# Performance work log

Hardware: AMD Instinct MI355X
Metric: run time of the kernel (lower is better)

Reference implementation:

```python
import jax, jax.numpy as jnp
import numpy as np

N, E, F_IN, HEADS, C_HEAD, HID, B, NCLS = 20000, 320000, 128, 2, 256, 512, 64, 38
EL = E + N  # edges with self-loops appended


def _bn(x, g, b, eps=1e-5):
    mu = jnp.mean(x, 0)
    var = jnp.mean((x - mu) ** 2, 0)
    return g * (x - mu) * jax.lax.rsqrt(var + eps) + b


def _gcn(x, W, b, src, dst):
    # src/dst already include self-loops; symmetric deg^-1/2 normalization (PyG GCNConv)
    h = x @ W                                             # [N, HID]
    deg = jax.ops.segment_sum(jnp.ones(EL, x.dtype), dst, N)
    norm = jax.lax.rsqrt(jnp.maximum(deg, 1.0))
    coef = norm[src] * norm[dst]                          # [EL]
    agg = jax.ops.segment_sum(h[src] * coef[:, None], dst, N)
    return agg + b


def _gat(x, W, a_src, a_dst, b, src, dst):
    # PyG GATConv, heads=2, concat: alpha = softmax_dst(leaky_relu(a_s.h_src + a_d.h_dst))
    h = (x @ W).reshape(N, HEADS, C_HEAD)
    as_n = jnp.sum(h * a_src, -1)                         # [N, HEADS]
    ad_n = jnp.sum(h * a_dst, -1)
    e = jax.nn.leaky_relu(as_n[src] + ad_n[dst], 0.2)     # [EL, HEADS]
    m = jax.ops.segment_max(e, dst, N)
    ex = jnp.exp(e - m[dst])
    s = jax.ops.segment_sum(ex, dst, N)
    alpha = ex / s[dst]                                   # [EL, HEADS]
    out = jax.ops.segment_sum(h[src] * alpha[:, :, None], dst, N)
    return out.reshape(N, HEADS * C_HEAD) + b


def setup_inputs() -> dict:
    key = jax.random.key(0)
    ks = jax.random.split(key, 40)
    x = jax.random.normal(ks[0], (N, F_IN), jnp.float32)
    edge_index = jax.random.randint(ks[1], (2, E), 0, N, jnp.int32)
    batch = jnp.sort(jax.random.randint(ks[2], (N,), 0, B, jnp.int32))

    def lin(k, fi, fo):
        bound = np.sqrt(6.0 / fi)
        return jax.random.uniform(k, (fi, fo), jnp.float32, -bound, bound)

    d = dict(x=x, edge_index=edge_index, batch=batch)
    # feature transform
    d['ft_W'] = lin(ks[3], F_IN, HID); d['ft_b'] = jnp.zeros(HID)
    d['ft_g'] = jnp.ones(HID); d['ft_be'] = jnp.zeros(HID)
    # GCN block
    d['gcn1_W'] = lin(ks[4], HID, HID); d['gcn1_b'] = jnp.zeros(HID)
    d['gbn1_g'] = jnp.ones(HID); d['gbn1_b'] = jnp.zeros(HID)
    d['gcn2_W'] = lin(ks[5], HID, HID); d['gcn2_b'] = jnp.zeros(HID)
    d['gbn2_g'] = jnp.ones(HID); d['gbn2_b'] = jnp.zeros(HID)
    # GAT block
    abound = np.sqrt(6.0 / HEADS)
    d['gat1_W'] = lin(ks[6], HID, HID)
    d['gat1_as'] = jax.random.uniform(ks[7], (HEADS, C_HEAD), jnp.float32, -abound, abound)
    d['gat1_ad'] = jax.random.uniform(ks[8], (HEADS, C_HEAD), jnp.float32, -abound, abound)
    d['gat1_b'] = jnp.zeros(HID)
    d['abn1_g'] = jnp.ones(HID); d['abn1_b'] = jnp.zeros(HID)
    d['gat2_W'] = lin(ks[9], HID, HID)
    d['gat2_as'] = jax.random.uniform(ks[10], (HEADS, C_HEAD), jnp.float32, -abound, abound)
    d['gat2_ad'] = jax.random.uniform(ks[11], (HEADS, C_HEAD), jnp.float32, -abound, abound)
    d['gat2_b'] = jnp.zeros(HID)
    d['abn2_g'] = jnp.ones(HID); d['abn2_b'] = jnp.zeros(HID)
    # classifier
    d['fc1_W'] = lin(ks[12], 2 * HID, HID); d['fc1_b'] = jnp.zeros(HID)
    d['cbn1_g'] = jnp.ones(HID); d['cbn1_b'] = jnp.zeros(HID)
    d['fc2_W'] = lin(ks[13], HID, HID // 2); d['fc2_b'] = jnp.zeros(HID // 2)
    d['cbn2_g'] = jnp.ones(HID // 2); d['cbn2_b'] = jnp.zeros(HID // 2)
    d['out_W'] = lin(ks[14], HID // 2, NCLS); d['out_b'] = jnp.zeros(NCLS)
    return d


def reference(x, edge_index, batch,
              ft_W, ft_b, ft_g, ft_be,
              gcn1_W, gcn1_b, gbn1_g, gbn1_b, gcn2_W, gcn2_b, gbn2_g, gbn2_b,
              gat1_W, gat1_as, gat1_ad, gat1_b, abn1_g, abn1_b,
              gat2_W, gat2_as, gat2_ad, gat2_b, abn2_g, abn2_b,
              fc1_W, fc1_b, cbn1_g, cbn1_b, fc2_W, fc2_b, cbn2_g, cbn2_b,
              out_W, out_b):
    loop = jnp.arange(N, dtype=edge_index.dtype)
    src = jnp.concatenate([edge_index[0], loop])
    dst = jnp.concatenate([edge_index[1], loop])

    # feature transform: Linear -> BN -> LeakyReLU(0.2)
    h = jax.nn.leaky_relu(_bn(x @ ft_W + ft_b, ft_g, ft_be), 0.2)
    # GCN block
    h = jax.nn.elu(_bn(_gcn(h, gcn1_W, gcn1_b, src, dst), gbn1_g, gbn1_b))
    h = jax.nn.elu(_bn(_gcn(h, gcn2_W, gcn2_b, src, dst), gbn2_g, gbn2_b))
    # GAT block
    h = jax.nn.elu(_bn(_gat(h, gat1_W, gat1_as, gat1_ad, gat1_b, src, dst), abn1_g, abn1_b))
    h = jax.nn.elu(_bn(_gat(h, gat2_W, gat2_as, gat2_ad, gat2_b, src, dst), abn2_g, abn2_b))
    # global mean+max pool over graphs
    cnt = jax.ops.segment_sum(jnp.ones(N, h.dtype), batch, B)
    mean_p = jax.ops.segment_sum(h, batch, B) / jnp.maximum(cnt, 1.0)[:, None]
    max_p = jax.ops.segment_max(h, batch, B)
    p = jnp.concatenate([mean_p, max_p], axis=1)           # [B, 1024]
    # classifier: fc1 -> bn -> fc2 -> bn -> leaky_relu -> out
    z = _bn(p @ fc1_W + fc1_b, cbn1_g, cbn1_b)
    z = _bn(z @ fc2_W + fc2_b, cbn2_g, cbn2_b)
    z = jax.nn.leaky_relu(z, 0.2)
    return z @ out_W + out_b                                # [B, NCLS]
```

## Files before the change

kernel.cpp:

```cpp
#include <hip/hip_runtime.h>

#define N_NODES 20000
#define N_EDGES 320000
#define EDG_ALL (N_EDGES + N_NODES)
#define F_IN 128
#define HID 512
#define NB 64
#define NCLS 38
#define M_PAD 20096
#define NBLK_SCAN ((N_NODES + 255) / 256)
#define BN_ROWS 16
#define BN_GRID ((N_NODES + BN_ROWS - 1) / BN_ROWS)
#define POOL_SPLIT 4

typedef short bf16x8 __attribute__((ext_vector_type(8)));
typedef float f32x4 __attribute__((ext_vector_type(4)));
typedef _Float16 f16;
typedef _Float16 f16x2 __attribute__((ext_vector_type(2)));

__device__ inline unsigned short f2bf(float f) {
  union { float f; unsigned u; } v; v.f = f;
  unsigned r = v.u + 0x7FFF + ((v.u >> 16) & 1);
  return (unsigned short)(r >> 16);
}

__device__ inline void split2(float f, unsigned short& h, unsigned short& l) {
  unsigned short hh = f2bf(f);
  union { unsigned u; float f; } vh; vh.u = ((unsigned)hh) << 16;
  h = hh;
  l = f2bf(f - vh.f);
}

__device__ inline void gload16(const void* g, void* l) {
  __builtin_amdgcn_global_load_lds(
      (const __attribute__((address_space(1))) unsigned int*)g,
      (__attribute__((address_space(3))) unsigned int*)l, 16, 0, 0);
}


__global__ void deg_count(const int* __restrict__ ei, int* __restrict__ deg) {
  int e = blockIdx.x * blockDim.x + threadIdx.x;
  if (e >= EDG_ALL) return;
  int d = (e < N_EDGES) ? ei[N_EDGES + e] : (e - N_EDGES);
  atomicAdd(&deg[d], 1);
}

__global__ void scan_p1(const int* __restrict__ deg, int* __restrict__ bsum) {
  __shared__ int sh[256];
  int b = blockIdx.x, t = threadIdx.x, i = b * 256 + t;
  sh[t] = (i < N_NODES) ? deg[i] : 0;
  __syncthreads();
  for (int o = 128; o > 0; o >>= 1) {
    if (t < o) sh[t] += sh[t + o];
    __syncthreads();
  }
  if (t == 0) bsum[b] = sh[0];
}

__global__ void scan_p2(const int* __restrict__ bsum, int* __restrict__ boff) {
  __shared__ int sh[128];
  int t = threadIdx.x;
  sh[t] = (t < NBLK_SCAN) ? bsum[t] : 0;
  __syncthreads();
  for (int o = 1; o < 128; o <<= 1) {
    int v = (t >= o) ? sh[t - o] : 0;
    __syncthreads();
    sh[t] += v;
    __syncthreads();
  }
  boff[t] = (t == 0) ? 0 : sh[t - 1];
}

__global__ void scan_p3(const int* __restrict__ deg, const int* __restrict__ boff,
                        int* __restrict__ row_ptr) {
  __shared__ int sh[256];
  int b = blockIdx.x, t = threadIdx.x, i = b * 256 + t;
  sh[t] = (i < N_NODES) ? deg[i] : 0;
  __syncthreads();
  for (int o = 1; o < 256; o <<= 1) {
    int v = (t >= o) ? sh[t - o] : 0;
    __syncthreads();
    sh[t] += v;
    __syncthreads();
  }
  if (i < N_NODES) row_ptr[i + 1] = boff[b] + sh[t];
  if (i == 0) row_ptr[0] = 0;
}

__global__ void compute_norm(const int* __restrict__ deg, float* __restrict__ norm) {
  int i = blockIdx.x * blockDim.x + threadIdx.x;
  if (i >= N_NODES) return;
  norm[i] = rsqrtf(fmaxf((float)deg[i], 1.f));
}

__global__ void fill_csr(const int* __restrict__ ei, int* __restrict__ cursor,
                         int* __restrict__ csr_src) {
  int e = blockIdx.x * blockDim.x + threadIdx.x;
  if (e >= EDG_ALL) return;
  int s, d;
  if (e < N_EDGES) { s = ei[e]; d = ei[N_EDGES + e]; }
  else { s = d = e - N_EDGES; }
  int pos = atomicAdd(&cursor[d], 1);
  csr_src[pos] = s;
}


__global__ void conv_split4(const float* __restrict__ in, unsigned short* __restrict__ hi,
                            unsigned short* __restrict__ lo, int n4) {
  int i = blockIdx.x * blockDim.x + threadIdx.x;
  if (i >= n4) return;
  float4 v = ((const float4*)in)[i];
  ushort4 h, l;
  split2(v.x, h.x, l.x); split2(v.y, h.y, l.y);
  split2(v.z, h.z, l.z); split2(v.w, h.w, l.w);
  ((ushort4*)hi)[i] = h;
  ((ushort4*)lo)[i] = l;
}

__global__ __launch_bounds__(256) void wtrans_split(const float* __restrict__ W,
                                                    unsigned short* __restrict__ WTh,
                                                    unsigned short* __restrict__ WTl,
                                                    int K, int N) {
  __shared__ float sh[32][33];
  int k0 = blockIdx.y * 32, n0 = blockIdx.x * 32;
  int r = threadIdx.x >> 5, c = threadIdx.x & 31;
#pragma unroll
  for (int i = 0; i < 4; ++i)
    sh[r + 8 * i][c] = W[(size_t)(k0 + r + 8 * i) * N + n0 + c];
  __syncthreads();
#pragma unroll
  for (int i = 0; i < 4; ++i) {
    unsigned short h, l;
    split2(sh[c][r + 8 * i], h, l);
    WTh[(size_t)(n0 + r + 8 * i) * K + k0 + c] = h;
    WTl[(size_t)(n0 + r + 8 * i) * K + k0 + c] = l;
  }
}

__global__ __launch_bounds__(256) void ftrans(const float* __restrict__ W,
                                              float* __restrict__ WT, int K, int N) {
  __shared__ float sh[32][33];
  int k0 = blockIdx.y * 32, n0 = blockIdx.x * 32;
  int r = threadIdx.x >> 5, c = threadIdx.x & 31;
#pragma unroll
  for (int i = 0; i < 4; ++i) {
    int k = k0 + r + 8 * i, n = n0 + c;
    sh[r + 8 * i][c] = (k < K && n < N) ? W[(size_t)k * N + n] : 0.f;
  }
  __syncthreads();
#pragma unroll
  for (int i = 0; i < 4; ++i) {
    int n = n0 + r + 8 * i, k = k0 + c;
    if (n < N && k < K) WT[(size_t)n * K + k] = sh[c][r + 8 * i];
  }
}


template <int K, typename OT>
__global__ __launch_bounds__(256) void mm_split(const unsigned short* __restrict__ Ah,
                                                const unsigned short* __restrict__ Al,
                                                const unsigned short* __restrict__ Bh,
                                                const unsigned short* __restrict__ Bl,
                                                const float* __restrict__ bias,
                                                OT* __restrict__ C) {
  __shared__ unsigned short AsH[4096], AsL[4096], BsH[4096], BsL[4096];
  const int t = threadIdx.x;
  const int wid = t >> 6, l = t & 63;
  const int row0 = blockIdx.y * 128;
  const int col0 = blockIdx.x * 128;
  const int wm = wid >> 1, wn = wid & 1;

  f32x4 acc[4][4];
#pragma unroll
  for (int m = 0; m < 4; ++m)
#pragma unroll
    for (int n = 0; n < 4; ++n)
#pragma unroll
      for (int q = 0; q < 4; ++q) acc[m][n][q] = 0.f;

  const size_t aoff = (size_t)(row0 + wid * 32 + (l >> 2)) * K + (l & 3) * 8;
  const size_t boff = (size_t)(col0 + wid * 32 + (l >> 2)) * K + (l & 3) * 8;
  const unsigned short* gAh0 = Ah + aoff; const unsigned short* gAh1 = gAh0 + (size_t)16 * K;
  const unsigned short* gAl0 = Al + aoff; const unsigned short* gAl1 = gAl0 + (size_t)16 * K;
  const unsigned short* gBh0 = Bh + boff; const unsigned short* gBh1 = gBh0 + (size_t)16 * K;
  const unsigned short* gBl0 = Bl + boff; const unsigned short* gBl1 = gBl0 + (size_t)16 * K;
  unsigned short* lAh0 = &AsH[(wid * 2 + 0) * 512];
  unsigned short* lAh1 = &AsH[(wid * 2 + 1) * 512];
  unsigned short* lAl0 = &AsL[(wid * 2 + 0) * 512];
  unsigned short* lAl1 = &AsL[(wid * 2 + 1) * 512];
  unsigned short* lBh0 = &BsH[(wid * 2 + 0) * 512];
  unsigned short* lBh1 = &BsH[(wid * 2 + 1) * 512];
  unsigned short* lBl0 = &BsL[(wid * 2 + 0) * 512];
  unsigned short* lBl1 = &BsL[(wid * 2 + 1) * 512];

  const int lr = l & 15, kq = (l >> 4) * 8;

  for (int kt = 0; kt < K / 32; ++kt) {
    const int ko = kt * 32;
    gload16(gAh0 + ko, lAh0);
    gload16(gAh1 + ko, lAh1);
    gload16(gAl0 + ko, lAl0);
    gload16(gAl1 + ko, lAl1);
    gload16(gBh0 + ko, lBh0);
    gload16(gBh1 + ko, lBh1);
    gload16(gBl0 + ko, lBl0);
    gload16(gBl1 + ko, lBl1);
    __syncthreads();
    bf16x8 ah[4], al[4], bh[4], bl[4];
#pragma unroll
    for (int m = 0; m < 4; ++m) {
      int ro = (wm * 64 + m * 16 + lr) * 32 + kq;
      ah[m] = *(const bf16x8*)&AsH[ro];
      al[m] = *(const bf16x8*)&AsL[ro];
    }
#pragma unroll
    for (int n = 0; n < 4; ++n) {
      int ro = (wn * 64 + n * 16 + lr) * 32 + kq;
      bh[n] = *(const bf16x8*)&BsH[ro];
      bl[n] = *(const bf16x8*)&BsL[ro];
    }
#pragma unroll
    for (int m = 0; m < 4; ++m)
#pragma unroll
      for (int n = 0; n < 4; ++n) {
        acc[m][n] = __builtin_amdgcn_mfma_f32_16x16x32_bf16(ah[m], bh[n], acc[m][n], 0, 0, 0);
        acc[m][n] = __builtin_amdgcn_mfma_f32_16x16x32_bf16(al[m], bh[n], acc[m][n], 0, 0, 0);
        acc[m][n] = __builtin_amdgcn_mfma_f32_16x16x32_bf16(ah[m], bl[n], acc[m][n], 0, 0, 0);
      }
    __syncthreads();
  }

  const int lg = l >> 4;
#pragma unroll
  for (int m = 0; m < 4; ++m) {
    int row = row0 + wm * 64 + m * 16 + lg * 4;
#pragma unroll
    for (int n = 0; n < 4; ++n) {
      int col = col0 + wn * 64 + n * 16 + lr;
      float bv = bias ? bias[col] : 0.f;
#pragma unroll
      for (int j = 0; j < 4; ++j)
        C[(size_t)(row + j) * HID + col] = (OT)(acc[m][n][j] + bv);
    }
  }
}


__global__ __launch_bounds__(256) void colstats(const float* __restrict__ X, int n,
                                                float* __restrict__ stats) {
  int t = threadIdx.x;
  int r0 = blockIdx.x * BN_ROWS;
  int r1 = min(r0 + BN_ROWS, n);
  float s0 = 0, q0 = 0, s1 = 0, q1 = 0;
  for (int r = r0; r < r1; ++r) {
    float a = X[(size_t)r * HID + t];
    float b = X[(size_t)r * HID + t + 256];
    s0 += a; q0 += a * a;
    s1 += b; q1 += b * b;
  }
  atomicAdd(&stats[t], s0);
  atomicAdd(&stats[t + 256], s1);
  atomicAdd(&stats[HID + t], q0);
  atomicAdd(&stats[HID + t + 256], q1);
}

__global__ __launch_bounds__(256) void bn_act(float* __restrict__ X, int n,
                                              const float* __restrict__ stats,
                                              const float* __restrict__ g,
                                              const float* __restrict__ b, int act,
                                              unsigned short* __restrict__ hio,
                                              unsigned short* __restrict__ loo,
                                              int writeX) {
  int t = threadIdx.x;
  int r0 = blockIdx.x * BN_ROWS;
  int r1 = min(r0 + BN_ROWS, n);
  float invn = 1.f / (float)n;
  float mu0 = stats[t] * invn, mu1 = stats[t + 256] * invn;
  float v0 = stats[HID + t] * invn - mu0 * mu0;
  float v1 = stats[HID + t + 256] * invn - mu1 * mu1;
  float sc0 = g[t] * rsqrtf(v0 + 1e-5f);
  float sc1 = g[t + 256] * rsqrtf(v1 + 1e-5f);
  float b0 = b[t], b1 = b[t + 256];
  for (int r = r0; r < r1; ++r) {
    float y0 = sc0 * (X[(size_t)r * HID + t] - mu0) + b0;
    float y1 = sc1 * (X[(size_t)r * HID + t + 256] - mu1) + b1;
    if (act == 1) {
      y0 = y0 > 0.f ? y0 : 0.2f * y0;
      y1 = y1 > 0.f ? y1 : 0.2f * y1;
    } else {
      y0 = y0 > 0.f ? y0 : expm1f(y0);
      y1 = y1 > 0.f ? y1 : expm1f(y1);
    }
    unsigned short h0, l0, h1, l1;
    split2(y0, h0, l0);
    split2(y1, h1, l1);
    hio[(size_t)r * HID + t] = h0;
    hio[(size_t)r * HID + t + 256] = h1;
    loo[(size_t)r * HID + t] = l0;
    loo[(size_t)r * HID + t + 256] = l1;
    if (writeX) {
      X[(size_t)r * HID + t] = y0;
      X[(size_t)r * HID + t + 256] = y1;
    }
  }
}


__global__ __launch_bounds__(256) void gcn_agg_h(
    const f16* __restrict__ h, const int* __restrict__ row_ptr,
    const int* __restrict__ csr_src, const float* __restrict__ norm,
    const float* __restrict__ bias, float* __restrict__ out) {
  int i = blockIdx.x;
  int t = threadIdx.x;
  int beg = row_ptr[i], end = row_ptr[i + 1];
  float ni = norm[i];
  const f16x2* h2 = (const f16x2*)h;
  float a0 = 0.f, a1 = 0.f;
  int e = beg;
  for (; e + 8 <= end; e += 8) {
    int s[8]; float c[8]; f16x2 v[8];
#pragma unroll
    for (int k = 0; k < 8; ++k) s[k] = csr_src[e + k];
#pragma unroll
    for (int k = 0; k < 8; ++k) c[k] = norm[s[k]] * ni;
#pragma unroll
    for (int k = 0; k < 8; ++k) v[k] = h2[(size_t)s[k] * 256 + t];
#pragma unroll
    for (int k = 0; k < 8; ++k) {
      a0 += c[k] * (float)v[k].x;
      a1 += c[k] * (float)v[k].y;
    }
  }
  for (; e < end; ++e) {
    int s = csr_src[e];
    float c = norm[s] * ni;
    f16x2 hv = h2[(size_t)s * 256 + t];
    a0 += c * (float)hv.x;
    a1 += c * (float)hv.y;
  }
  float2 bv = ((const float2*)bias)[t];
  float2 o; o.x = a0 + bv.x; o.y = a1 + bv.y;
  ((float2*)out)[(size_t)i * 256 + t] = o;
}


__device__ inline float wave_sum(float v) {
#pragma unroll
  for (int o = 32; o > 0; o >>= 1) v += __shfl_down(v, o);
  return v;
}
__device__ inline float wave_max(float v) {
#pragma unroll
  for (int o = 32; o > 0; o >>= 1) v = fmaxf(v, __shfl_down(v, o));
  return v;
}

__global__ __launch_bounds__(256) void gat_prep_h(
    const f16* __restrict__ h, const float* __restrict__ a_src,
    const float* __restrict__ a_dst, float* __restrict__ asn, float* __restrict__ adn) {
  int i = blockIdx.x;
  int t = threadIdx.x;
  f16x2 hv = ((const f16x2*)h)[(size_t)i * 256 + t];
  float2 as2 = ((const float2*)a_src)[t];
  float2 ad2 = ((const float2*)a_dst)[t];
  float h0 = (float)hv.x, h1 = (float)hv.y;
  float s = h0 * as2.x + h1 * as2.y;
  float d = h0 * ad2.x + h1 * ad2.y;
  s = wave_sum(s); d = wave_sum(d);
  __shared__ float red[4][2];
  int w = t >> 6;
  if ((t & 63) == 0) { red[w][0] = s; red[w][1] = d; }
  __syncthreads();
  if (t == 0) {
    asn[2 * i]     = red[0][0] + red[1][0];
    asn[2 * i + 1] = red[2][0] + red[3][0];
    adn[2 * i]     = red[0][1] + red[1][1];
    adn[2 * i + 1] = red[2][1] + red[3][1];
  }
}

__global__ __launch_bounds__(256) void gat_agg_h(
    const f16* __restrict__ h, const int* __restrict__ row_ptr,
    const int* __restrict__ csr_src, const float* __restrict__ asn,
    const float* __restrict__ adn, const float* __restrict__ bias,
    float* __restrict__ out) {
  int i = blockIdx.x;
  int t = threadIdx.x;
  int beg = row_ptr[i], end = row_ptr[i + 1];
  float ad0 = adn[2 * i], ad1 = adn[2 * i + 1];

  float m0 = -3.4e38f, m1 = -3.4e38f;
#pragma unroll 4
  for (int e = beg + t; e < end; e += 256) {
    int s = csr_src[e];
    float e0 = asn[2 * s] + ad0;     e0 = e0 > 0.f ? e0 : 0.2f * e0;
    float e1 = asn[2 * s + 1] + ad1; e1 = e1 > 0.f ? e1 : 0.2f * e1;
    m0 = fmaxf(m0, e0); m1 = fmaxf(m1, e1);
  }
  __shared__ float red0[4], red1[4];
  float r0 = wave_max(m0), r1 = wave_max(m1);
  if ((t & 63) == 0) { red0[t >> 6] = r0; red1[t >> 6] = r1; }
  __syncthreads();
  float M0 = fmaxf(fmaxf(red0[0], red0[1]), fmaxf(red0[2], red0[3]));
  float M1 = fmaxf(fmaxf(red1[0], red1[1]), fmaxf(red1[2], red1[3]));
  __syncthreads();

  __shared__ float w0s[64], w1s[64];
  __shared__ int ss[64];
  __shared__ float sS0, sS1;
  const f16x2* h2 = (const f16x2*)h;
  float acc0 = 0.f, acc1 = 0.f;
  float sw0 = 0.f, sw1 = 0.f;
  for (int c = beg; c < end; c += 64) {
    int nc = min(64, end - c);
    if (t < nc) {
      int s = csr_src[c + t];
      ss[t] = s;
      float e0 = asn[2 * s] + ad0;     e0 = e0 > 0.f ? e0 : 0.2f * e0;
      float e1 = asn[2 * s + 1] + ad1; e1 = e1 > 0.f ? e1 : 0.2f * e1;
      float w0 = expf(e0 - M0), w1 = expf(e1 - M1);
      w0s[t] = w0; w1s[t] = w1;
      sw0 += w0; sw1 += w1;
    }
    __syncthreads();
    int j = 0;
    for (; j + 8 <= nc; j += 8) {
      int s[8]; f16x2 v[8]; float u[8];
#pragma unroll
      for (int k = 0; k < 8; ++k) s[k] = ss[j + k];
#pragma unroll
      for (int k = 0; k < 8; ++k) v[k] = h2[(size_t)s[k] * 256 + t];
#pragma unroll
      for (int k = 0; k < 8; ++k) u[k] = (t < 128) ? w0s[j + k] : w1s[j + k];
#pragma unroll
      for (int k = 0; k < 8; ++k) {
        acc0 += u[k] * (float)v[k].x;
        acc1 += u[k] * (float)v[k].y;
      }
    }
    for (; j < nc; ++j) {
      int s = ss[j];
      f16x2 hv = h2[(size_t)s * 256 + t];
      float w = (t < 128) ? w0s[j] : w1s[j];
      acc0 += w * (float)hv.x;
      acc1 += w * (float)hv.y;
    }
    __syncthreads();
  }
  if (t < 64) {
    float a = wave_sum(sw0);
    float b = wave_sum(sw1);
    if (t == 0) { sS0 = a; sS1 = b; }
  }
  __syncthreads();
  float iS = (t < 128) ? (1.f / sS0) : (1.f / sS1);
  float2 bv = ((const float2*)bias)[t];
  float2 o; o.x = acc0 * iS + bv.x; o.y = acc1 * iS + bv.y;
  ((float2*)out)[(size_t)i * 256 + t] = o;
}


__global__ void graph_starts(const int* __restrict__ batch, int* __restrict__ start) {
  int i = blockIdx.x * blockDim.x + threadIdx.x;
  if (i >= N_NODES) return;
  int b = batch[i];
  int bp = (i == 0) ? -1 : batch[i - 1];
  for (int g = bp + 1; g <= b; ++g) start[g] = i;
  if (i == N_NODES - 1) {
    for (int g = b + 1; g <= NB; ++g) start[g] = N_NODES;
  }
}

__global__ __launch_bounds__(512) void pool_part(const float* __restrict__ h,
                                                 const int* __restrict__ start,
                                                 float* __restrict__ pp_sum,
                                                 float* __restrict__ pp_max) {
  int b = blockIdx.x, ch = blockIdx.y, t = threadIdx.x;
  int s = start[b], e = start[b + 1];
  int len = e - s;
  int c0 = s + (len * ch) / POOL_SPLIT;
  int c1 = s + (len * (ch + 1)) / POOL_SPLIT;
  float sum = 0.f, mx = -3.4e38f;
  int r = c0;
  for (; r + 4 <= c1; r += 4) {
    float v0 = h[(size_t)(r + 0) * HID + t];
    float v1 = h[(size_t)(r + 1) * HID + t];
    float v2 = h[(size_t)(r + 2) * HID + t];
    float v3 = h[(size_t)(r + 3) * HID + t];
    sum += v0 + v1 + v2 + v3;
    mx = fmaxf(mx, fmaxf(fmaxf(v0, v1), fmaxf(v2, v3)));
  }
  for (; r < c1; ++r) {
    float v = h[(size_t)r * HID + t];
    sum += v; mx = fmaxf(mx, v);
  }
  pp_sum[((size_t)b * POOL_SPLIT + ch) * HID + t] = sum;
  pp_max[((size_t)b * POOL_SPLIT + ch) * HID + t] = mx;
}

__global__ __launch_bounds__(512) void pool_comb(const float* __restrict__ pp_sum,
                                                 const float* __restrict__ pp_max,
                                                 const int* __restrict__ start,
                                                 float* __restrict__ p) {
  int b = blockIdx.x, t = threadIdx.x;
  float sum = 0.f, mx = -3.4e38f;
#pragma unroll
  for (int ch = 0; ch < POOL_SPLIT; ++ch) {
    sum += pp_sum[((size_t)b * POOL_SPLIT + ch) * HID + t];
    mx = fmaxf(mx, pp_max[((size_t)b * POOL_SPLIT + ch) * HID + t]);
  }
  float cnt = (float)(start[b + 1] - start[b]);
  p[b * 1024 + t] = sum / fmaxf(cnt, 1.f);
  p[b * 1024 + 512 + t] = mx;
}


__global__ __launch_bounds__(256) void fc_wave(const float* __restrict__ A,
                                               const float* __restrict__ WT,
                                               const float* __restrict__ bias,
                                               float* __restrict__ C, int K, int Ncol) {
  int r = blockIdx.x;
  int wid = threadIdx.x >> 6, l = threadIdx.x & 63;
  int c = blockIdx.y * 4 + wid;
  if (c >= Ncol) return;
  const float* a = A + (size_t)r * K;
  const float* w = WT + (size_t)c * K;
  float s = 0.f;
  for (int k = l; k < K; k += 64) s += a[k] * w[k];
#pragma unroll
  for (int o = 32; o > 0; o >>= 1) s += __shfl_down(s, o);
  if (l == 0) C[(size_t)r * Ncol + c] = s + bias[c];
}

__global__ void bn_small(float* __restrict__ X, int R, int C,
                         const float* __restrict__ g, const float* __restrict__ b, int act) {
  int c = blockIdx.x * blockDim.x + threadIdx.x;
  if (c >= C) return;
  float s = 0.f, q = 0.f;
  for (int r = 0; r < R; ++r) {
    float v = X[r * C + c];
    s += v; q += v * v;
  }
  float mu = s / R;
  float var = q / R - mu * mu;
  float sc = g[c] * rsqrtf(var + 1e-5f);
  float bb = b[c];
  for (int r = 0; r < R; ++r) {
    float v = sc * (X[r * C + c] - mu) + bb;
    if (act == 1) v = v > 0.f ? v : 0.2f * v;
    X[r * C + c] = v;
  }
}


extern "C" void kernel_launch(void* const* d_in, const int* in_sizes, int n_in,
                              void* d_out, int out_size, void* d_ws, size_t ws_size,
                              hipStream_t stream) {
  const float* x      = (const float*)d_in[0];
  const int*   ei     = (const int*)d_in[1];
  const int*   batch  = (const int*)d_in[2];
  const float* ft_W   = (const float*)d_in[3];
  const float* ft_b   = (const float*)d_in[4];
  const float* ft_g   = (const float*)d_in[5];
  const float* ft_be  = (const float*)d_in[6];
  const float* gcn1_W = (const float*)d_in[7];
  const float* gcn1_b = (const float*)d_in[8];
  const float* gbn1_g = (const float*)d_in[9];
  const float* gbn1_b = (const float*)d_in[10];
  const float* gcn2_W = (const float*)d_in[11];
  const float* gcn2_b = (const float*)d_in[12];
  const float* gbn2_g = (const float*)d_in[13];
  const float* gbn2_b = (const float*)d_in[14];
  const float* gat1_W = (const float*)d_in[15];
  const float* gat1_as= (const float*)d_in[16];
  const float* gat1_ad= (const float*)d_in[17];
  const float* gat1_b = (const float*)d_in[18];
  const float* abn1_g = (const float*)d_in[19];
  const float* abn1_b = (const float*)d_in[20];
  const float* gat2_W = (const float*)d_in[21];
  const float* gat2_as= (const float*)d_in[22];
  const float* gat2_ad= (const float*)d_in[23];
  const float* gat2_b = (const float*)d_in[24];
  const float* abn2_g = (const float*)d_in[25];
  const float* abn2_b = (const float*)d_in[26];
  const float* fc1_W  = (const float*)d_in[27];
  const float* fc1_b  = (const float*)d_in[28];
  const float* cbn1_g = (const float*)d_in[29];
  const float* cbn1_b = (const float*)d_in[30];
  const float* fc2_W  = (const float*)d_in[31];
  const float* fc2_b  = (const float*)d_in[32];
  const float* cbn2_g = (const float*)d_in[33];
  const float* cbn2_b = (const float*)d_in[34];
  const float* out_W  = (const float*)d_in[35];
  const float* out_b  = (const float*)d_in[36];

  char* ws = (char*)d_ws;
  size_t off = 0;
  auto alloc = [&](size_t bytes) -> void* {
    void* p = ws + off;
    off = (off + bytes + 255) & ~(size_t)255;
    return p;
  };

  float* buf0 = (float*)alloc((size_t)N_NODES * HID * 4);
  float* buf1 = (float*)alloc((size_t)M_PAD * HID * 4);
  unsigned short* ahi = (unsigned short*)alloc((size_t)N_NODES * HID * 2);
  unsigned short* alo = (unsigned short*)alloc((size_t)N_NODES * HID * 2);
  unsigned short* wh_ft = (unsigned short*)alloc((size_t)HID * F_IN * 2);
  unsigned short* wl_ft = (unsigned short*)alloc((size_t)HID * F_IN * 2);
  unsigned short* wh_g1 = (unsigned short*)alloc((size_t)HID * HID * 2);
  unsigned short* wl_g1 = (unsigned short*)alloc((size_t)HID * HID * 2);
  unsigned short* wh_g2 = (unsigned short*)alloc((size_t)HID * HID * 2);
  unsigned short* wl_g2 = (unsigned short*)alloc((size_t)HID * HID * 2);
  unsigned short* wh_a1 = (unsigned short*)alloc((size_t)HID * HID * 2);
  unsigned short* wl_a1 = (unsigned short*)alloc((size_t)HID * HID * 2);
  unsigned short* wh_a2 = (unsigned short*)alloc((size_t)HID * HID * 2);
  unsigned short* wl_a2 = (unsigned short*)alloc((size_t)HID * HID * 2);
  float* fc1t = (float*)alloc((size_t)512 * 1024 * 4);
  float* fc2t = (float*)alloc((size_t)256 * 512 * 4);
  float* outt = (float*)alloc((size_t)NCLS * 256 * 4);
  int*   row_ptr = (int*)alloc((N_NODES + 1) * 4);
  int*   cursor  = (int*)alloc(N_NODES * 4);
  int*   deg     = (int*)alloc(N_NODES * 4);
  int*   csr_src = (int*)alloc(EDG_ALL * 4);
  float* norm    = (float*)alloc(N_NODES * 4);
  float* asn     = (float*)alloc(N_NODES * 2 * 4);
  float* adn     = (float*)alloc(N_NODES * 2 * 4);
  float* stats   = (float*)alloc(1024 * 4);
  int*   bsum    = (int*)alloc(128 * 4);
  int*   boff    = (int*)alloc(128 * 4);
  int*   start   = (int*)alloc((NB + 1) * 4);
  float* p       = (float*)alloc(NB * 1024 * 4);
  float* pp_sum  = (float*)alloc((size_t)NB * POOL_SPLIT * HID * 4);
  float* pp_max  = (float*)alloc((size_t)NB * POOL_SPLIT * HID * 4);
  float* z1      = (float*)alloc(NB * HID * 4);
  float* z2      = (float*)alloc(NB * 256 * 4);
  unsigned short* xhi = (unsigned short*)buf0;
  unsigned short* xlo = xhi + (size_t)N_NODES * F_IN;
  f16* hbuf = (f16*)buf1;

  const dim3 blk256(256);
  const dim3 mmGrid(4, M_PAD / 128);

  hipMemsetAsync(deg, 0, N_NODES * 4, stream);
  deg_count<<<(EDG_ALL + 255) / 256, blk256, 0, stream>>>(ei, deg);
  scan_p1<<<NBLK_SCAN, blk256, 0, stream>>>(deg, bsum);
  scan_p2<<<1, 128, 0, stream>>>(bsum, boff);
  scan_p3<<<NBLK_SCAN, blk256, 0, stream>>>(deg, boff, row_ptr);
  compute_norm<<<(N_NODES + 255) / 256, blk256, 0, stream>>>(deg, norm);
  hipMemcpyAsync(cursor, row_ptr, N_NODES * 4, hipMemcpyDeviceToDevice, stream);
  fill_csr<<<(EDG_ALL + 255) / 256, blk256, 0, stream>>>(ei, cursor, csr_src);

  wtrans_split<<<dim3(HID / 32, F_IN / 32), blk256, 0, stream>>>(ft_W, wh_ft, wl_ft, F_IN, HID);
  wtrans_split<<<dim3(HID / 32, HID / 32), blk256, 0, stream>>>(gcn1_W, wh_g1, wl_g1, HID, HID);
  wtrans_split<<<dim3(HID / 32, HID / 32), blk256, 0, stream>>>(gcn2_W, wh_g2, wl_g2, HID, HID);
  wtrans_split<<<dim3(HID / 32, HID / 32), blk256, 0, stream>>>(gat1_W, wh_a1, wl_a1, HID, HID);
  wtrans_split<<<dim3(HID / 32, HID / 32), blk256, 0, stream>>>(gat2_W, wh_a2, wl_a2, HID, HID);
  ftrans<<<dim3(512 / 32, 1024 / 32), blk256, 0, stream>>>(fc1_W, fc1t, 1024, 512);
  ftrans<<<dim3(256 / 32, 512 / 32), blk256, 0, stream>>>(fc2_W, fc2t, 512, 256);
  ftrans<<<dim3((NCLS + 31) / 32, 256 / 32), blk256, 0, stream>>>(out_W, outt, 256, NCLS);

  conv_split4<<<(N_NODES * F_IN / 4 + 255) / 256, blk256, 0, stream>>>(x, xhi, xlo, N_NODES * F_IN / 4);
  mm_split<F_IN, float><<<mmGrid, blk256, 0, stream>>>(xhi, xlo, wh_ft, wl_ft, ft_b, buf1);
  hipMemsetAsync(stats, 0, 1024 * 4, stream);
  colstats<<<BN_GRID, blk256, 0, stream>>>(buf1, N_NODES, stats);
  bn_act<<<BN_GRID, blk256, 0, stream>>>(buf1, N_NODES, stats, ft_g, ft_be, 1, ahi, alo, 0);

  mm_split<HID, f16><<<mmGrid, blk256, 0, stream>>>(ahi, alo, wh_g1, wl_g1, nullptr, hbuf);
  gcn_agg_h<<<N_NODES, blk256, 0, stream>>>(hbuf, row_ptr, csr_src, norm, gcn1_b, buf0);
  hipMemsetAsync(stats, 0, 1024 * 4, stream);
  colstats<<<BN_GRID, blk256, 0, stream>>>(buf0, N_NODES, stats);
  bn_act<<<BN_GRID, blk256, 0, stream>>>(buf0, N_NODES, stats, gbn1_g, gbn1_b, 2, ahi, alo, 0);

  mm_split<HID, f16><<<mmGrid, blk256, 0, stream>>>(ahi, alo, wh_g2, wl_g2, nullptr, hbuf);
  gcn_agg_h<<<N_NODES, blk256, 0, stream>>>(hbuf, row_ptr, csr_src, norm, gcn2_b, buf0);
  hipMemsetAsync(stats, 0, 1024 * 4, stream);
  colstats<<<BN_GRID, blk256, 0, stream>>>(buf0, N_NODES, stats);
  bn_act<<<BN_GRID, blk256, 0, stream>>>(buf0, N_NODES, stats, gbn2_g, gbn2_b, 2, ahi, alo, 0);

  mm_split<HID, f16><<<mmGrid, blk256, 0, stream>>>(ahi, alo, wh_a1, wl_a1, nullptr, hbuf);
  gat_prep_h<<<N_NODES, blk256, 0, stream>>>(hbuf, gat1_as, gat1_ad, asn, adn);
  gat_agg_h<<<N_NODES, blk256, 0, stream>>>(hbuf, row_ptr, csr_src, asn, adn, gat1_b, buf0);
  hipMemsetAsync(stats, 0, 1024 * 4, stream);
  colstats<<<BN_GRID, blk256, 0, stream>>>(buf0, N_NODES, stats);
  bn_act<<<BN_GRID, blk256, 0, stream>>>(buf0, N_NODES, stats, abn1_g, abn1_b, 2, ahi, alo, 0);

  mm_split<HID, f16><<<mmGrid, blk256, 0, stream>>>(ahi, alo, wh_a2, wl_a2, nullptr, hbuf);
  gat_prep_h<<<N_NODES, blk256, 0, stream>>>(hbuf, gat2_as, gat2_ad, asn, adn);
  gat_agg_h<<<N_NODES, blk256, 0, stream>>>(hbuf, row_ptr, csr_src, asn, adn, gat2_b, buf0);
  hipMemsetAsync(stats, 0, 1024 * 4, stream);
  colstats<<<BN_GRID, blk256, 0, stream>>>(buf0, N_NODES, stats);
  bn_act<<<BN_GRID, blk256, 0, stream>>>(buf0, N_NODES, stats, abn2_g, abn2_b, 2, ahi, alo, 1);

  graph_starts<<<(N_NODES + 255) / 256, blk256, 0, stream>>>(batch, start);
  pool_part<<<dim3(NB, POOL_SPLIT), dim3(512), 0, stream>>>(buf0, start, pp_sum, pp_max);
  pool_comb<<<NB, dim3(512), 0, stream>>>(pp_sum, pp_max, start, p);

  fc_wave<<<dim3(NB, 128), blk256, 0, stream>>>(p, fc1t, fc1_b, z1, 1024, 512);
  bn_small<<<2, blk256, 0, stream>>>(z1, NB, 512, cbn1_g, cbn1_b, 0);
  fc_wave<<<dim3(NB, 64), blk256, 0, stream>>>(z1, fc2t, fc2_b, z2, 512, 256);
  bn_small<<<1, blk256, 0, stream>>>(z2, NB, 256, cbn2_g, cbn2_b, 1);
  fc_wave<<<dim3(NB, 10), blk256, 0, stream>>>(z2, outt, out_b, (float*)d_out, 256, NCLS);

  (void)in_sizes; (void)n_in; (void)out_size; (void)ws_size;
}
```

Measured before the change: 930.0 us.

## Aggregate GCN/GAT with one wavefront per node and 16-byte feature loads

Rewrites the GCN and GAT neighbor aggregation kernels to map one 64-lane wavefront per destination node (4 nodes per block) instead of one 256-thread block per node. Each lane loads 8 fp16 features at once. The GAT kernel drops its shared-memory staging and block barriers and recomputes edge weights per lane using wave shuffles. The intent is to cut per-node block overhead and synchronisation and to widen memory transactions. In exchange, each lane redundantly reads indices and computes exp per edge. colstats and bn_act are also switched to float2-vectorized accesses; their stats layout stays consistent because both change together.

```diff
diff --git a/kernel.cpp b/kernel.cpp
--- a/kernel.cpp
+++ b/kernel.cpp
@@ -16,7 +16,7 @@
 typedef short bf16x8 __attribute__((ext_vector_type(8)));
 typedef float f32x4 __attribute__((ext_vector_type(4)));
 typedef _Float16 f16;
-typedef _Float16 f16x2 __attribute__((ext_vector_type(2)));
+typedef _Float16 f16x8 __attribute__((ext_vector_type(8)));
 
 __device__ inline unsigned short f2bf(float f) {
   union { float f; unsigned u; } v; v.f = f;
@@ -252,16 +252,16 @@
   int r0 = blockIdx.x * BN_ROWS;
   int r1 = min(r0 + BN_ROWS, n);
   float s0 = 0, q0 = 0, s1 = 0, q1 = 0;
+  const float2* X2 = (const float2*)X;
   for (int r = r0; r < r1; ++r) {
-    float a = X[(size_t)r * HID + t];
-    float b = X[(size_t)r * HID + t + 256];
-    s0 += a; q0 += a * a;
-    s1 += b; q1 += b * b;
-  }
-  atomicAdd(&stats[t], s0);
-  atomicAdd(&stats[t + 256], s1);
-  atomicAdd(&stats[HID + t], q0);
-  atomicAdd(&stats[HID + t + 256], q1);
+    float2 v = X2[(size_t)r * 256 + t];
+    s0 += v.x; q0 += v.x * v.x;
+    s1 += v.y; q1 += v.y * v.y;
+  }
+  atomicAdd(&stats[2 * t], s0);
+  atomicAdd(&stats[2 * t + 1], s1);
+  atomicAdd(&stats[HID + 2 * t], q0);
+  atomicAdd(&stats[HID + 2 * t + 1], q1);
 }
 
 __global__ __launch_bounds__(256) void bn_act(float* __restrict__ X, int n,
@@ -275,15 +275,20 @@
   int r0 = blockIdx.x * BN_ROWS;
   int r1 = min(r0 + BN_ROWS, n);
   float invn = 1.f / (float)n;
-  float mu0 = stats[t] * invn, mu1 = stats[t + 256] * invn;
-  float v0 = stats[HID + t] * invn - mu0 * mu0;
-  float v1 = stats[HID + t + 256] * invn - mu1 * mu1;
-  float sc0 = g[t] * rsqrtf(v0 + 1e-5f);
-  float sc1 = g[t + 256] * rsqrtf(v1 + 1e-5f);
-  float b0 = b[t], b1 = b[t + 256];
+  float mu0 = stats[2 * t] * invn, mu1 = stats[2 * t + 1] * invn;
+  float v0 = stats[HID + 2 * t] * invn - mu0 * mu0;
+  float v1 = stats[HID + 2 * t + 1] * invn - mu1 * mu1;
+  float2 gg = ((const float2*)g)[t];
+  float2 bb = ((const float2*)b)[t];
+  float sc0 = gg.x * rsqrtf(v0 + 1e-5f);
+  float sc1 = gg.y * rsqrtf(v1 + 1e-5f);
+  float2* X2 = (float2*)X;
+  ushort2* H2 = (ushort2*)hio;
+  ushort2* L2p = (ushort2*)loo;
   for (int r = r0; r < r1; ++r) {
-    float y0 = sc0 * (X[(size_t)r * HID + t] - mu0) + b0;
-    float y1 = sc1 * (X[(size_t)r * HID + t + 256] - mu1) + b1;
+    float2 xv = X2[(size_t)r * 256 + t];
+    float y0 = sc0 * (xv.x - mu0) + bb.x;
+    float y1 = sc1 * (xv.y - mu1) + bb.y;
     if (act == 1) {
       y0 = y0 > 0.f ? y0 : 0.2f * y0;
       y1 = y1 > 0.f ? y1 : 0.2f * y1;
@@ -294,53 +299,54 @@
     unsigned short h0, l0, h1, l1;
     split2(y0, h0, l0);
     split2(y1, h1, l1);
-    hio[(size_t)r * HID + t] = h0;
-    hio[(size_t)r * HID + t + 256] = h1;
-    loo[(size_t)r * HID + t] = l0;
-    loo[(size_t)r * HID + t + 256] = l1;
+    ushort2 hh; hh.x = h0; hh.y = h1;
+    ushort2 ll; ll.x = l0; ll.y = l1;
+    H2[(size_t)r * 256 + t] = hh;
+    L2p[(size_t)r * 256 + t] = ll;
     if (writeX) {
-      X[(size_t)r * HID + t] = y0;
-      X[(size_t)r * HID + t + 256] = y1;
+      float2 yv; yv.x = y0; yv.y = y1;
+      X2[(size_t)r * 256 + t] = yv;
     }
   }
 }
 
 
-__global__ __launch_bounds__(256) void gcn_agg_h(
+__global__ __launch_bounds__(256) void gcn_agg_w(
     const f16* __restrict__ h, const int* __restrict__ row_ptr,
     const int* __restrict__ csr_src, const float* __restrict__ norm,
     const float* __restrict__ bias, float* __restrict__ out) {
-  int i = blockIdx.x;
-  int t = threadIdx.x;
-  int beg = row_ptr[i], end = row_ptr[i + 1];
-  float ni = norm[i];
-  const f16x2* h2 = (const f16x2*)h;
-  float a0 = 0.f, a1 = 0.f;
+  int node = blockIdx.x * 4 + (threadIdx.x >> 6);
+  int l = threadIdx.x & 63;
+  int beg = row_ptr[node], end = row_ptr[node + 1];
+  float ni = norm[node];
+  const f16x8* h8 = (const f16x8*)h;
+  float acc[8] = {};
   int e = beg;
-  for (; e + 8 <= end; e += 8) {
-    int s[8]; float c[8]; f16x2 v[8];
-#pragma unroll
-    for (int k = 0; k < 8; ++k) s[k] = csr_src[e + k];
-#pragma unroll
-    for (int k = 0; k < 8; ++k) c[k] = norm[s[k]] * ni;
-#pragma unroll
-    for (int k = 0; k < 8; ++k) v[k] = h2[(size_t)s[k] * 256 + t];
-#pragma unroll
-    for (int k = 0; k < 8; ++k) {
-      a0 += c[k] * (float)v[k].x;
-      a1 += c[k] * (float)v[k].y;
-    }
+  for (; e + 4 <= end; e += 4) {
+    int s0 = csr_src[e], s1 = csr_src[e + 1], s2 = csr_src[e + 2], s3 = csr_src[e + 3];
+    float c0 = norm[s0] * ni, c1 = norm[s1] * ni, c2 = norm[s2] * ni, c3 = norm[s3] * ni;
+    f16x8 v0 = h8[(size_t)s0 * 64 + l];
+    f16x8 v1 = h8[(size_t)s1 * 64 + l];
+    f16x8 v2 = h8[(size_t)s2 * 64 + l];
+    f16x8 v3 = h8[(size_t)s3 * 64 + l];
+#pragma unroll
+    for (int k = 0; k < 8; ++k)
+      acc[k] += c0 * (float)v0[k] + c1 * (float)v1[k] + c2 * (float)v2[k] + c3 * (float)v3[k];
   }
   for (; e < end; ++e) {
     int s = csr_src[e];
     float c = norm[s] * ni;
-    f16x2 hv = h2[(size_t)s * 256 + t];
-    a0 += c * (float)hv.x;
-    a1 += c * (float)hv.y;
-  }
-  float2 bv = ((const float2*)bias)[t];
-  float2 o; o.x = a0 + bv.x; o.y = a1 + bv.y;
-  ((float2*)out)[(size_t)i * 256 + t] = o;
+    f16x8 v = h8[(size_t)s * 64 + l];
+#pragma unroll
+    for (int k = 0; k < 8; ++k) acc[k] += c * (float)v[k];
+  }
+  float4 b0 = ((const float4*)bias)[l * 2];
+  float4 b1 = ((const float4*)bias)[l * 2 + 1];
+  float4 o0, o1;
+  o0.x = acc[0] + b0.x; o0.y = acc[1] + b0.y; o0.z = acc[2] + b0.z; o0.w = acc[3] + b0.w;
+  o1.x = acc[4] + b1.x; o1.y = acc[5] + b1.y; o1.z = acc[6] + b1.z; o1.w = acc[7] + b1.w;
+  ((float4*)out)[(size_t)node * 128 + l * 2] = o0;
+  ((float4*)out)[(size_t)node * 128 + l * 2 + 1] = o1;
 }
 
 
@@ -349,12 +355,8 @@
   for (int o = 32; o > 0; o >>= 1) v += __shfl_down(v, o);
   return v;
 }
-__device__ inline float wave_max(float v) {
-#pragma unroll
-  for (int o = 32; o > 0; o >>= 1) v = fmaxf(v, __shfl_down(v, o));
-  return v;
-}
-
+
+typedef _Float16 f16x2 __attribute__((ext_vector_type(2)));
 __global__ __launch_bounds__(256) void gat_prep_h(
     const f16* __restrict__ h, const float* __restrict__ a_src,
     const float* __restrict__ a_dst, float* __restrict__ asn, float* __restrict__ adn) {
@@ -379,84 +381,76 @@
   }
 }
 
-__global__ __launch_bounds__(256) void gat_agg_h(
+__device__ inline float lrelu(float v) { return v > 0.f ? v : 0.2f * v; }
+
+__global__ __launch_bounds__(256) void gat_agg_w(
     const f16* __restrict__ h, const int* __restrict__ row_ptr,
     const int* __restrict__ csr_src, const float* __restrict__ asn,
     const float* __restrict__ adn, const float* __restrict__ bias,
     float* __restrict__ out) {
-  int i = blockIdx.x;
-  int t = threadIdx.x;
-  int beg = row_ptr[i], end = row_ptr[i + 1];
-  float ad0 = adn[2 * i], ad1 = adn[2 * i + 1];
+  int node = blockIdx.x * 4 + (threadIdx.x >> 6);
+  int l = threadIdx.x & 63;
+  int beg = row_ptr[node], end = row_ptr[node + 1];
+  float ad0 = adn[2 * node], ad1 = adn[2 * node + 1];
 
   float m0 = -3.4e38f, m1 = -3.4e38f;
-#pragma unroll 4
-  for (int e = beg + t; e < end; e += 256) {
+  for (int e = beg + l; e < end; e += 64) {
     int s = csr_src[e];
-    float e0 = asn[2 * s] + ad0;     e0 = e0 > 0.f ? e0 : 0.2f * e0;
-    float e1 = asn[2 * s + 1] + ad1; e1 = e1 > 0.f ? e1 : 0.2f * e1;
-    m0 = fmaxf(m0, e0); m1 = fmaxf(m1, e1);
-  }
-  __shared__ float red0[4], red1[4];
-  float r0 = wave_max(m0), r1 = wave_max(m1);
-  if ((t & 63) == 0) { red0[t >> 6] = r0; red1[t >> 6] = r1; }
-  __syncthreads();
-  float M0 = fmaxf(fmaxf(red0[0], red0[1]), fmaxf(red0[2], red0[3]));
-  float M1 = fmaxf(fmaxf(red1[0], red1[1]), fmaxf(red1[2], red1[3]));
-  __syncthreads();
-
-  __shared__ float w0s[64], w1s[64];
-  __shared__ int ss[64];
-  __shared__ float sS0, sS1;
-  const f16x2* h2 = (const f16x2*)h;
-  float acc0 = 0.f, acc1 = 0.f;
+    m0 = fmaxf(m0, lrelu(asn[2 * s] + ad0));
+    m1 = fmaxf(m1, lrelu(asn[2 * s + 1] + ad1));
+  }
+#pragma unroll
+  for (int o = 32; o > 0; o >>= 1) {
+    m0 = fmaxf(m0, __shfl_down(m0, o));
+    m1 = fmaxf(m1, __shfl_down(m1, o));
+  }
+  float M0 = __shfl(m0, 0);
+  float M1 = __shfl(m1, 0);
+
+  const f16x8* h8 = (const f16x8*)h;
+  float acc[8] = {};
   float sw0 = 0.f, sw1 = 0.f;
-  for (int c = beg; c < end; c += 64) {
-    int nc = min(64, end - c);
-    if (t < nc) {
-      int s = csr_src[c + t];
-      ss[t] = s;
-      float e0 = asn[2 * s] + ad0;     e0 = e0 > 0.f ? e0 : 0.2f * e0;
-      float e1 = asn[2 * s + 1] + ad1; e1 = e1 > 0.f ? e1 : 0.2f * e1;
-      float w0 = expf(e0 - M0), w1 = expf(e1 - M1);
-      w0s[t] = w0; w1s[t] = w1;
-      sw0 += w0; sw1 += w1;
-    }
-    __syncthreads();
-    int j = 0;
-    for (; j + 8 <= nc; j += 8) {
-      int s[8]; f16x2 v[8]; float u[8];
-#pragma unroll
-      for (int k = 0; k < 8; ++k) s[k] = ss[j + k];
-#pragma unroll
-      for (int k = 0; k < 8; ++k) v[k] = h2[(size_t)s[k] * 256 + t];
-#pragma unroll
-      for (int k = 0; k < 8; ++k) u[k] = (t < 128) ? w0s[j + k] : w1s[j + k];
-#pragma unroll
-      for (int k = 0; k < 8; ++k) {
-        acc0 += u[k] * (float)v[k].x;
-        acc1 += u[k] * (float)v[k].y;
-      }
-    }
-    for (; j < nc; ++j) {
-      int s = ss[j];
-      f16x2 hv = h2[(size_t)s * 256 + t];
-      float w = (t < 128) ? w0s[j] : w1s[j];
-      acc0 += w * (float)hv.x;
-      acc1 += w * (float)hv.y;
-    }
-    __syncthreads();
-  }
-  if (t < 64) {
-    float a = wave_sum(sw0);
-    float b = wave_sum(sw1);
-    if (t == 0) { sS0 = a; sS1 = b; }
-  }
-  __syncthreads();
-  float iS = (t < 128) ? (1.f / sS0) : (1.f / sS1);
-  float2 bv = ((const float2*)bias)[t];
-  float2 o; o.x = acc0 * iS + bv.x; o.y = acc1 * iS + bv.y;
-  ((float2*)out)[(size_t)i * 256 + t] = o;
+  int e = beg;
+  for (; e + 4 <= end; e += 4) {
+    int s0 = csr_src[e], s1 = csr_src[e + 1], s2 = csr_src[e + 2], s3 = csr_src[e + 3];
+    float w00 = expf(lrelu(asn[2 * s0] + ad0) - M0), w01 = expf(lrelu(asn[2 * s0 + 1] + ad1) - M1);
+    float w10 = expf(lrelu(asn[2 * s1] + ad0) - M0), w11 = expf(lrelu(asn[2 * s1 + 1] + ad1) - M1);
+    float w20 = expf(lrelu(asn[2 * s2] + ad0) - M0), w21 = expf(lrelu(asn[2 * s2 + 1] + ad1) - M1);
+    float w30 = expf(lrelu(asn[2 * s3] + ad0) - M0), w31 = expf(lrelu(asn[2 * s3 + 1] + ad1) - M1);
+    sw0 += w00 + w10 + w20 + w30;
+    sw1 += w01 + w11 + w21 + w31;
+    f16x8 v0 = h8[(size_t)s0 * 64 + l];
+    f16x8 v1 = h8[(size_t)s1 * 64 + l];
+    f16x8 v2 = h8[(size_t)s2 * 64 + l];
+    f16x8 v3 = h8[(size_t)s3 * 64 + l];
+    float u0 = (l < 32) ? w00 : w01;
+    float u1 = (l < 32) ? w10 : w11;
+    float u2 = (l < 32) ? w20 : w21;
+    float u3 = (l < 32) ? w30 : w31;
+#pragma unroll
+    for (int k = 0; k < 8; ++k)
+      acc[k] += u0 * (float)v0[k] + u1 * (float)v1[k] + u2 * (float)v2[k] + u3 * (float)v3[k];
+  }
+  for (; e < end; ++e) {
+    int s = csr_src[e];
+    float w0 = expf(lrelu(asn[2 * s] + ad0) - M0);
+    float w1 = expf(lrelu(asn[2 * s + 1] + ad1) - M1);
+    sw0 += w0; sw1 += w1;
+    f16x8 v = h8[(size_t)s * 64 + l];
+    float u = (l < 32) ? w0 : w1;
+#pragma unroll
+    for (int k = 0; k < 8; ++k) acc[k] += u * (float)v[k];
+  }
+  float iS = (l < 32) ? (1.f / sw0) : (1.f / sw1);
+  float4 b0 = ((const float4*)bias)[l * 2];
+  float4 b1 = ((const float4*)bias)[l * 2 + 1];
+  float4 o0, o1;
+  o0.x = acc[0] * iS + b0.x; o0.y = acc[1] * iS + b0.y;
+  o0.z = acc[2] * iS + b0.z; o0.w = acc[3] * iS + b0.w;
+  o1.x = acc[4] * iS + b1.x; o1.y = acc[5] * iS + b1.y;
+  o1.z = acc[6] * iS + b1.z; o1.w = acc[7] * iS + b1.w;
+  ((float4*)out)[(size_t)node * 128 + l * 2] = o0;
+  ((float4*)out)[(size_t)node * 128 + l * 2 + 1] = o1;
 }
 
 
@@ -641,6 +635,7 @@
 
   const dim3 blk256(256);
   const dim3 mmGrid(4, M_PAD / 128);
+  const int aggGrid = N_NODES / 4;
 
   hipMemsetAsync(deg, 0, N_NODES * 4, stream);
   deg_count<<<(EDG_ALL + 255) / 256, blk256, 0, stream>>>(ei, deg);
@@ -667,27 +662,27 @@
   bn_act<<<BN_GRID, blk256, 0, stream>>>(buf1, N_NODES, stats, ft_g, ft_be, 1, ahi, alo, 0);
 
   mm_split<HID, f16><<<mmGrid, blk256, 0, stream>>>(ahi, alo, wh_g1, wl_g1, nullptr, hbuf);
-  gcn_agg_h<<<N_NODES, blk256, 0, stream>>>(hbuf, row_ptr, csr_src, norm, gcn1_b, buf0);
+  gcn_agg_w<<<aggGrid, blk256, 0, stream>>>(hbuf, row_ptr, csr_src, norm, gcn1_b, buf0);
   hipMemsetAsync(stats, 0, 1024 * 4, stream);
   colstats<<<BN_GRID, blk256, 0, stream>>>(buf0, N_NODES, stats);
   bn_act<<<BN_GRID, blk256, 0, stream>>>(buf0, N_NODES, stats, gbn1_g, gbn1_b, 2, ahi, alo, 0);
 
   mm_split<HID, f16><<<mmGrid, blk256, 0, stream>>>(ahi, alo, wh_g2, wl_g2, nullptr, hbuf);
-  gcn_agg_h<<<N_NODES, blk256, 0, stream>>>(hbuf, row_ptr, csr_src, norm, gcn2_b, buf0);
+  gcn_agg_w<<<aggGrid, blk256, 0, stream>>>(hbuf, row_ptr, csr_src, norm, gcn2_b, buf0);
   hipMemsetAsync(stats, 0, 1024 * 4, stream);
   colstats<<<BN_GRID, blk256, 0, stream>>>(buf0, N_NODES, stats);
   bn_act<<<BN_GRID, blk256, 0, stream>>>(buf0, N_NODES, stats, gbn2_g, gbn2_b, 2, ahi, alo, 0);
 
   mm_split<HID, f16><<<mmGrid, blk256, 0, stream>>>(ahi, alo, wh_a1, wl_a1, nullptr, hbuf);
   gat_prep_h<<<N_NODES, blk256, 0, stream>>>(hbuf, gat1_as, gat1_ad, asn, adn);
-  gat_agg_h<<<N_NODES, blk256, 0, stream>>>(hbuf, row_ptr, csr_src, asn, adn, gat1_b, buf0);
+  gat_agg_w<<<aggGrid, blk256, 0, stream>>>(hbuf, row_ptr, csr_src, asn, adn, gat1_b, buf0);
   hipMemsetAsync(stats, 0, 1024 * 4, stream);
   colstats<<<BN_GRID, blk256, 0, stream>>>(buf0, N_NODES, stats);
   bn_act<<<BN_GRID, blk256, 0, stream>>>(buf0, N_NODES, stats, abn1_g, abn1_b, 2, ahi, alo, 0);
 
   mm_split<HID, f16><<<mmGrid, blk256, 0, stream>>>(ahi, alo, wh_a2, wl_a2, nullptr, hbuf);
   gat_prep_h<<<N_NODES, blk256, 0, stream>>>(hbuf, gat2_as, gat2_ad, asn, adn);
-  gat_agg_h<<<N_NODES, blk256, 0, stream>>>(hbuf, row_ptr, csr_src, asn, adn, gat2_b, buf0);
+  gat_agg_w<<<aggGrid, blk256, 0, stream>>>(hbuf, row_ptr, csr_src, asn, adn, gat2_b, buf0);
   hipMemsetAsync(stats, 0, 1024 * 4, stream);
   colstats<<<BN_GRID, blk256, 0, stream>>>(buf0, N_NODES, stats);
   bn_act<<<BN_GRID, blk256, 0, stream>>>(buf0, N_NODES, stats, abn2_g, abn2_b, 2, ahi, alo, 1);
```

Result: slower. 1.058 ms (+13.8%).
